# Optimization experiments

Hardware: AMD Instinct MI355X
Metric: run time of the kernel (lower is better)

Reference implementation:

```python
import jax, jax.numpy as jnp
import numpy as np

N_NODES = 10000
N_EDGES = 160000
IN_F = 16
D = 512
N_GRAPHS = 64
N_OUT = 18
BN_EPS = 1e-5


def setup_inputs() -> dict:
    key = jax.random.key(0)
    ks = jax.random.split(key, 16)
    inp = {}
    inp["x"] = jax.random.normal(ks[0], (N_NODES, IN_F), dtype=jnp.float32)
    inp["edge_index"] = jax.random.randint(ks[1], (2, N_EDGES), 0, N_NODES, dtype=jnp.int32)
    inp["batch"] = jnp.sort(jax.random.randint(ks[2], (N_NODES,), 0, N_GRAPHS, dtype=jnp.int32))
    s_in = 1.0 / np.sqrt(IN_F)
    s_d = 1.0 / np.sqrt(D)
    # layer 1 MLP (Linear(IN_F,D) -> ReLU -> Linear(D,D))
    inp["W1a"] = jax.random.uniform(ks[3], (IN_F, D), jnp.float32, -s_in, s_in)
    inp["b1a"] = jnp.zeros((D,), jnp.float32)
    inp["W1b"] = jax.random.uniform(ks[4], (D, D), jnp.float32, -s_d, s_d)
    inp["b1b"] = jnp.zeros((D,), jnp.float32)
    # layers 2-5 stacked MLPs
    inp["Wa"] = jax.random.uniform(ks[5], (4, D, D), jnp.float32, -s_d, s_d)
    inp["ba"] = jnp.zeros((4, D), jnp.float32)
    inp["Wb"] = jax.random.uniform(ks[6], (4, D, D), jnp.float32, -s_d, s_d)
    inp["bb"] = jnp.zeros((4, D), jnp.float32)
    # batchnorm affine params for the 5 BN layers
    inp["bn_gamma"] = jnp.ones((5, D), jnp.float32)
    inp["bn_beta"] = jnp.zeros((5, D), jnp.float32)
    # final fc1 and logits head
    inp["Wfc"] = jax.random.uniform(ks[7], (D, D), jnp.float32, -s_d, s_d)
    inp["bfc"] = jnp.zeros((D,), jnp.float32)
    inp["Wlog"] = 0.01 * jax.random.normal(ks[8], (D, N_OUT), jnp.float32)
    inp["blog"] = jnp.zeros((N_OUT,), jnp.float32)
    return inp


def _gin_agg(x, src, dst):
    # GIN with eps=0: (1+eps)*x + sum_{j in N(i)} x_j  (messages src -> dst)
    msg = x[src]  # [E, D] gather
    agg = jax.ops.segment_sum(msg, dst, num_segments=N_NODES)
    return x + agg


def _mlp(h, Wa, ba, Wb, bb):
    return jax.nn.relu(h @ Wa + ba) @ Wb + bb


def _bn(h, gamma, beta):
    # BatchNorm1d training-mode: batch stats over node dim
    mean = jnp.mean(h, axis=0)
    var = jnp.var(h, axis=0)
    return (h - mean) * (gamma * jax.lax.rsqrt(var + BN_EPS)) + beta


def reference(x, edge_index, batch, W1a, b1a, W1b, b1b, Wa, ba, Wb, bb,
              bn_gamma, bn_beta, Wfc, bfc, Wlog, blog):
    src, dst = edge_index[0], edge_index[1]
    # conv1
    h = jax.nn.relu(_mlp(_gin_agg(x, src, dst), W1a, b1a, W1b, b1b))
    h = _bn(h, bn_gamma[0], bn_beta[0])
    # conv2..conv5
    for i in range(4):
        h = jax.nn.relu(_mlp(_gin_agg(h, src, dst), Wa[i], ba[i], Wb[i], bb[i]))
        h = _bn(h, bn_gamma[i + 1], bn_beta[i + 1])
    # global_mean_pool over graphs
    sums = jax.ops.segment_sum(h, batch, num_segments=N_GRAPHS)
    counts = jax.ops.segment_sum(jnp.ones((N_NODES,), jnp.float32), batch, num_segments=N_GRAPHS)
    pooled = sums / jnp.maximum(counts, 1.0)[:, None]  # [G, D]
    feats = jnp.tanh(pooled @ Wfc + bfc)
    logits = feats @ Wlog + blog  # [G, N_OUT]
    return logits
```

## Files before the change

### kernel.cpp

```cpp
#include <hip/hip_runtime.h>

#define NODES 10000
#define EDGES 160000
#define INF_ 16
#define DD 512
#define GRAPHS 64
#define NOUT 18
#define BN_EPS 1e-5f
#define NBUCK 8

using u16 = unsigned short;
typedef __attribute__((ext_vector_type(8))) _Float16 f16x8;
typedef __attribute__((ext_vector_type(4))) float f32x4;

__device__ __forceinline__ float h2f(u16 u) {
  union { u16 u; _Float16 h; } v; v.u = u; return (float)v.h;
}
__device__ __forceinline__ u16 f2h(float f) {
  union { u16 u; _Float16 h; } v; v.h = (_Float16)f; return v.u;
}
__device__ __forceinline__ void add8(uint4 u, float* a) {
  a[0] += h2f((u16)(u.x & 0xffff)); a[1] += h2f((u16)(u.x >> 16));
  a[2] += h2f((u16)(u.y & 0xffff)); a[3] += h2f((u16)(u.y >> 16));
  a[4] += h2f((u16)(u.z & 0xffff)); a[5] += h2f((u16)(u.z >> 16));
  a[6] += h2f((u16)(u.w & 0xffff)); a[7] += h2f((u16)(u.w >> 16));
}
__device__ __forceinline__ unsigned int pk(float a, float b) {
  return (unsigned int)f2h(a) | ((unsigned int)f2h(b) << 16);
}
__device__ __forceinline__ int lower_bound_dev(const int* __restrict__ batch, int g) {
  int lo = 0, hi = NODES;
  while (lo < hi) { int m = (lo + hi) >> 1; if (batch[m] < g) lo = m + 1; else hi = m; }
  return lo;
}
__device__ __forceinline__ int lds_m(int row, int byte) {
  return (row * 1152 + (byte ^ ((row & 7) << 4))) >> 1;
}

__global__ __launch_bounds__(256) void k_prep(int* __restrict__ cur, float* __restrict__ bg,
                                              const float* __restrict__ W1b, const float* __restrict__ Wa,
                                              const float* __restrict__ Wb, u16* __restrict__ Wf) {
  __shared__ float tile[32][33];
  int b = blockIdx.x;
  int t = threadIdx.x;
  if (b < 288) {
    bg[b * 256 + t] = 0.f;
    return;
  }
  if (b < 328) {
    int i = (b - 288) * 256 + t;
    if (i < NODES) cur[i] = 0;
    return;
  }
  int wb = b - 328;
  int nb = wb & 15, kb = (wb >> 4) & 15, z = wb >> 8;
  const float* src = (z == 0) ? W1b : (z <= 4 ? Wa + (size_t)(z - 1) * DD * DD
                                              : Wb + (size_t)(z - 5) * DD * DD);
  int tx = t & 31, ty = t >> 5;
#pragma unroll
  for (int i = 0; i < 4; ++i)
    tile[ty + 8 * i][tx] = src[(size_t)(kb * 32 + ty + 8 * i) * DD + nb * 32 + tx];
  __syncthreads();
  u16* dst = Wf + (size_t)z * 262144;
#pragma unroll
  for (int p = 0; p < 4; ++p) {
    int i = t + 256 * p;
    int ntl = i >> 9;
    int rem = i & 511;
    int kl = ((rem >> 3) & 3) * 8 + (rem & 7);
    int nl = ntl * 16 + (rem >> 5);
    dst[(size_t)((nb * 2 + ntl) * 16 + kb) * 512 + rem] = f2h(tile[kl][nl]);
  }
}

__global__ void k_count(const int* __restrict__ dst, int* __restrict__ cnt) {
  int e = blockIdx.x * 256 + threadIdx.x;
  if (e < EDGES) atomicAdd(&cnt[dst[e]], 1);
}

__global__ __launch_bounds__(1024) void k_scan(int* __restrict__ cnt, int* __restrict__ rowptr) {
  __shared__ int s[1024];
  int t = threadIdx.x;
  int base = t * 10;
  int c[10]; int sum = 0;
#pragma unroll
  for (int i = 0; i < 10; ++i) {
    int idx = base + i;
    c[i] = (idx < NODES) ? cnt[idx] : 0;
    if (idx < NODES) cnt[idx] = 0;
    sum += c[i];
  }
  s[t] = sum; __syncthreads();
  for (int off = 1; off < 1024; off <<= 1) {
    int v = s[t];
    int a = (t >= off) ? s[t - off] : 0;
    __syncthreads();
    s[t] = v + a;
    __syncthreads();
  }
  int run = (t == 0) ? 0 : s[t - 1];
#pragma unroll
  for (int i = 0; i < 10; ++i) { int idx = base + i; if (idx < NODES) rowptr[idx] = run; run += c[i]; }
  if (t == 1023) rowptr[NODES] = s[1023];
}

__global__ void k_fill(const int* __restrict__ src, const int* __restrict__ dst,
                       const int* __restrict__ rowptr, int* __restrict__ cur, int* __restrict__ col) {
  int e = blockIdx.x * 256 + threadIdx.x;
  if (e < EDGES) {
    int d = dst[e];
    int p = atomicAdd(&cur[d], 1);
    col[rowptr[d] + p] = src[e];
  }
}

__global__ __launch_bounds__(256) void k_l1(const float* __restrict__ x, const int* __restrict__ rowptr,
                                            const int* __restrict__ col, const float* __restrict__ W1a,
                                            const float* __restrict__ b1a, u16* __restrict__ out) {
  __shared__ float sh0[16][17];
  int t = threadIdx.x;
  int nl = t >> 4, ch = t & 15;
  int node = blockIdx.x * 16 + nl;
  float acc = x[node * INF_ + ch];
  int r1 = rowptr[node + 1];
  for (int idx = rowptr[node]; idx < r1; ++idx)
    acc += x[col[idx] * INF_ + ch];
  sh0[nl][ch] = acc;
  __syncthreads();
#pragma unroll
  for (int p = 0; p < 2; ++p) {
    int c = t + 256 * p;
    float wreg[16];
#pragma unroll
    for (int k = 0; k < 16; ++k) wreg[k] = W1a[k * DD + c];
    float bv = b1a[c];
#pragma unroll
    for (int r = 0; r < 16; ++r) {
      float s = bv;
#pragma unroll
      for (int k = 0; k < 16; ++k) s = fmaf(sh0[r][k], wreg[k], s);
      out[(size_t)(blockIdx.x * 16 + r) * DD + c] = f2h(fmaxf(s, 0.f));
    }
  }
}

__global__ __launch_bounds__(256) void k_gath(const u16* __restrict__ Hin, const int* __restrict__ rowptr,
                                              const int* __restrict__ col, const float* __restrict__ statsIn,
                                              const float* __restrict__ gamma, const float* __restrict__ beta,
                                              u16* __restrict__ Tout) {
  __shared__ float ssc[512], ssh[512];
  int t = threadIdx.x;
#pragma unroll
  for (int r = 0; r < 2; ++r) {
    int c = t + r * 256;
    float s = 0.f, qv = 0.f;
#pragma unroll
    for (int b = 0; b < NBUCK; ++b) {
      s += statsIn[b * 1024 + c];
      qv += statsIn[b * 1024 + 512 + c];
    }
    float mean = s * (1.f / NODES);
    float var = qv * (1.f / NODES) - mean * mean;
    float sc = gamma[c] * rsqrtf(var + BN_EPS);
    ssc[c] = sc;
    ssh[c] = beta[c] - mean * sc;
  }
  __syncthreads();

  int lane = t & 63;
  int node = blockIdx.x * 4 + (t >> 6);
  int c8 = lane * 8;
  const u16* hp = Hin + c8;
  float4 scA = *(const float4*)(ssc + c8), scB = *(const float4*)(ssc + c8 + 4);
  float4 shA = *(const float4*)(ssh + c8), shB = *(const float4*)(ssh + c8 + 4);
  float acc[8];
  {
    uint4 sv = *(const uint4*)(hp + (size_t)node * DD);
    acc[0] = h2f((u16)(sv.x & 0xffff)); acc[1] = h2f((u16)(sv.x >> 16));
    acc[2] = h2f((u16)(sv.y & 0xffff)); acc[3] = h2f((u16)(sv.y >> 16));
    acc[4] = h2f((u16)(sv.z & 0xffff)); acc[5] = h2f((u16)(sv.z >> 16));
    acc[6] = h2f((u16)(sv.w & 0xffff)); acc[7] = h2f((u16)(sv.w >> 16));
  }
  int r0 = rowptr[node], r1 = rowptr[node + 1];
  int idx = r0;
  for (; idx + 7 < r1; idx += 8) {
    int j0 = col[idx], j1 = col[idx + 1], j2 = col[idx + 2], j3 = col[idx + 3];
    int j4 = col[idx + 4], j5 = col[idx + 5], j6 = col[idx + 6], j7 = col[idx + 7];
    uint4 a = *(const uint4*)(hp + (size_t)j0 * DD);
    uint4 b = *(const uint4*)(hp + (size_t)j1 * DD);
    uint4 c = *(const uint4*)(hp + (size_t)j2 * DD);
    uint4 d = *(const uint4*)(hp + (size_t)j3 * DD);
    uint4 e = *(const uint4*)(hp + (size_t)j4 * DD);
    uint4 f = *(const uint4*)(hp + (size_t)j5 * DD);
    uint4 g = *(const uint4*)(hp + (size_t)j6 * DD);
    uint4 h = *(const uint4*)(hp + (size_t)j7 * DD);
    add8(a, acc); add8(b, acc); add8(c, acc); add8(d, acc);
    add8(e, acc); add8(f, acc); add8(g, acc); add8(h, acc);
  }
  for (; idx + 3 < r1; idx += 4) {
    int j0 = col[idx], j1 = col[idx + 1], j2 = col[idx + 2], j3 = col[idx + 3];
    uint4 a = *(const uint4*)(hp + (size_t)j0 * DD);
    uint4 b = *(const uint4*)(hp + (size_t)j1 * DD);
    uint4 c = *(const uint4*)(hp + (size_t)j2 * DD);
    uint4 d = *(const uint4*)(hp + (size_t)j3 * DD);
    add8(a, acc); add8(b, acc); add8(c, acc); add8(d, acc);
  }
  for (; idx < r1; ++idx) {
    uint4 a = *(const uint4*)(hp + (size_t)col[idx] * DD);
    add8(a, acc);
  }
  float nn = (float)(r1 - r0 + 1);
  uint4 o;
  o.x = pk(scA.x * acc[0] + nn * shA.x, scA.y * acc[1] + nn * shA.y);
  o.y = pk(scA.z * acc[2] + nn * shA.z, scA.w * acc[3] + nn * shA.w);
  o.z = pk(scB.x * acc[4] + nn * shB.x, scB.y * acc[5] + nn * shB.y);
  o.w = pk(scB.z * acc[6] + nn * shB.z, scB.w * acc[7] + nn * shB.w);
  *(uint4*)(Tout + (size_t)node * DD + c8) = o;
}

__device__ __forceinline__ void gemm_tile(const u16* At, const u16* __restrict__ Wz,
                                          int wave, int q, int r16, f32x4 (&acc)[4][2]) {
  const u16* wp = Wz + (size_t)(wave * 2) * 16 * 512 + (r16 * 4 + q) * 8;
#pragma unroll
  for (int ks = 0; ks < 16; ++ks) {
    f16x8 af[4], bh[2];
#pragma unroll
    for (int mt = 0; mt < 4; ++mt)
      af[mt] = *(const f16x8*)(At + lds_m(mt * 16 + r16, ks * 64 + q * 16));
#pragma unroll
    for (int nt = 0; nt < 2; ++nt)
      bh[nt] = *(const f16x8*)(wp + (size_t)(nt * 16 + ks) * 512);
#pragma unroll
    for (int mt = 0; mt < 4; ++mt)
#pragma unroll
      for (int nt = 0; nt < 2; ++nt)
        acc[mt][nt] = __builtin_amdgcn_mfma_f32_16x16x32_f16(af[mt], bh[nt], acc[mt][nt], 0, 0, 0);
  }
}

template <int TWO>
__global__ __launch_bounds__(1024, 4) void k_mlp(const u16* __restrict__ Ag,
    const u16* __restrict__ WzA, const float* __restrict__ bA,
    const u16* __restrict__ WzB, const float* __restrict__ bB,
    u16* __restrict__ Hout, float* __restrict__ statsB) {
  __shared__ __align__(16) u16 At[64 * 576];
  const int T = threadIdx.x;
  const int M0 = blockIdx.x * 64;
#pragma unroll
  for (int p = 0; p < 4; ++p) {
    int idx = p * 1024 + T;
    int row = idx >> 6, cq = idx & 63;
    uint4 v = make_uint4(0u, 0u, 0u, 0u);
    if (M0 + row < NODES) v = *(const uint4*)(Ag + (size_t)(M0 + row) * DD + cq * 8);
    *(uint4*)(At + lds_m(row, cq * 16)) = v;
  }
  __syncthreads();
  const int lane = T & 63, wave = T >> 6;
  const int q = lane >> 4, r16 = lane & 15;
  const int wn = wave * 32;
  if (TWO) {
    f32x4 acc[4][2] = {};
    gemm_tile(At, WzA, wave, q, r16, acc);
    __syncthreads();
#pragma unroll
    for (int nt = 0; nt < 2; ++nt) {
      int c = wn + nt * 16 + r16;
      float bv = bA[c];
#pragma unroll
      for (int mt = 0; mt < 4; ++mt)
#pragma unroll
        for (int rr = 0; rr < 4; ++rr)
          At[lds_m(mt * 16 + q * 4 + rr, c * 2)] = f2h(fmaxf(acc[mt][nt][rr] + bv, 0.f));
    }
    __syncthreads();
  }
  f32x4 acc[4][2] = {};
  gemm_tile(At, WzB, wave, q, r16, acc);
  float colS[2] = {}, colQ[2] = {};
#pragma unroll
  for (int nt = 0; nt < 2; ++nt) {
    int c = wn + nt * 16 + r16;
    float bv = bB[c];
#pragma unroll
    for (int mt = 0; mt < 4; ++mt) {
#pragma unroll
      for (int rr = 0; rr < 4; ++rr) {
        int row = M0 + mt * 16 + q * 4 + rr;
        if (row < NODES) {
          float v = fmaxf(acc[mt][nt][rr] + bv, 0.f);
          Hout[(size_t)row * DD + c] = f2h(v);
          colS[nt] += v; colQ[nt] += v * v;
        }
      }
    }
  }
#pragma unroll
  for (int nt = 0; nt < 2; ++nt) {
    colS[nt] += __shfl_xor(colS[nt], 16); colS[nt] += __shfl_xor(colS[nt], 32);
    colQ[nt] += __shfl_xor(colQ[nt], 16); colQ[nt] += __shfl_xor(colQ[nt], 32);
  }
  if (q == 0) {
    float* sb = statsB + (size_t)(blockIdx.x & (NBUCK - 1)) * 1024;
#pragma unroll
    for (int nt = 0; nt < 2; ++nt) {
      int c = wn + nt * 16 + r16;
      atomicAdd(&sb[c], colS[nt]);
      atomicAdd(&sb[512 + c], colQ[nt]);
    }
  }
}

__global__ __launch_bounds__(128) void k_pool_part(const u16* __restrict__ h, const int* __restrict__ batch,
                                                   float* __restrict__ gsum) {
  int g = blockIdx.x;
  int s = blockIdx.y;
  int c4 = threadIdx.x * 4;
  int r0 = lower_bound_dev(batch, g);
  int r1 = lower_bound_dev(batch, g + 1);
  int cnt = r1 - r0;
  int len = (cnt + 7) >> 3;
  int rs = r0 + s * len;
  int re = min(rs + len, r1);
  if (rs >= re) return;
  float4 acc = make_float4(0.f, 0.f, 0.f, 0.f);
  for (int r = rs; r < re; ++r) {
    ushort4 v = *(const ushort4*)(h + (size_t)r * DD + c4);
    acc.x += h2f(v.x); acc.y += h2f(v.y); acc.z += h2f(v.z); acc.w += h2f(v.w);
  }
  atomicAdd(&gsum[g * DD + c4 + 0], acc.x);
  atomicAdd(&gsum[g * DD + c4 + 1], acc.y);
  atomicAdd(&gsum[g * DD + c4 + 2], acc.z);
  atomicAdd(&gsum[g * DD + c4 + 3], acc.w);
}

__global__ __launch_bounds__(256) void k_headf(const float* __restrict__ gsum, const int* __restrict__ batch,
                                               const float* __restrict__ stats,
                                               const float* __restrict__ gamma, const float* __restrict__ beta,
                                               const float* __restrict__ Wfc, const float* __restrict__ bfc,
                                               float* __restrict__ feats) {
  __shared__ float pv[512];
  __shared__ float red[4][64];
  int g = blockIdx.x;
  int t = threadIdx.x;
  int r0 = lower_bound_dev(batch, g);
  int r1 = lower_bound_dev(batch, g + 1);
  float inv = 1.f / fmaxf((float)(r1 - r0), 1.f);
#pragma unroll
  for (int r = 0; r < 2; ++r) {
    int c = t + r * 256;
    float s = 0.f, qv = 0.f;
#pragma unroll
    for (int b = 0; b < NBUCK; ++b) {
      s += stats[b * 1024 + c];
      qv += stats[b * 1024 + 512 + c];
    }
    float mean = s * (1.f / NODES);
    float var = qv * (1.f / NODES) - mean * mean;
    float sc = gamma[c] * rsqrtf(var + BN_EPS);
    float sh = beta[c] - mean * sc;
    pv[c] = gsum[g * DD + c] * inv * sc + sh;
  }
  __syncthreads();
  int colc = blockIdx.y * 64 + (t & 63);
  int kc = t >> 6;
  float p = 0.f;
  int k0 = kc * 128;
  for (int k = k0; k < k0 + 128; ++k)
    p = fmaf(pv[k], Wfc[k * DD + colc], p);
  red[kc][t & 63] = p;
  __syncthreads();
  if (t < 64) {
    int c = blockIdx.y * 64 + t;
    float v = red[0][t] + red[1][t] + red[2][t] + red[3][t] + bfc[c];
    feats[g * DD + c] = tanhf(v);
  }
}

__global__ __launch_bounds__(64) void k_logits2(const float* __restrict__ feats, const float* __restrict__ Wlog,
                                                const float* __restrict__ blog, float* __restrict__ out) {
  int g = blockIdx.x, o = blockIdx.y;
  int lane = threadIdx.x;
  float p = 0.f;
  for (int k = lane; k < DD; k += 64)
    p = fmaf(feats[g * DD + k], Wlog[k * NOUT + o], p);
#pragma unroll
  for (int off = 32; off > 0; off >>= 1)
    p += __shfl_down(p, off);
  if (lane == 0) out[g * NOUT + o] = p + blog[o];
}

extern "C" void kernel_launch(void* const* d_in, const int* in_sizes, int n_in,
                              void* d_out, int out_size, void* d_ws, size_t ws_size,
                              hipStream_t stream) {
  const float* x = (const float*)d_in[0];
  const int* ei = (const int*)d_in[1];
  const int* batch = (const int*)d_in[2];
  const float* W1a = (const float*)d_in[3];
  const float* b1a = (const float*)d_in[4];
  const float* W1b = (const float*)d_in[5];
  const float* b1b = (const float*)d_in[6];
  const float* Wa = (const float*)d_in[7];
  const float* ba = (const float*)d_in[8];
  const float* Wb = (const float*)d_in[9];
  const float* bb = (const float*)d_in[10];
  const float* bng = (const float*)d_in[11];
  const float* bnb = (const float*)d_in[12];
  const float* Wfc = (const float*)d_in[13];
  const float* bfc = (const float*)d_in[14];
  const float* Wlog = (const float*)d_in[15];
  const float* blog = (const float*)d_in[16];
  float* out = (float*)d_out;

  const int* src = ei;
  const int* dstp = ei + EDGES;

  char* w = (char*)d_ws;
  int* rowptr  = (int*)(w);
  int* cur     = (int*)(w + 40192);
  int* col     = (int*)(w + 80384);
  float* bns   = (float*)(w + 720384);
  float* gsum  = (float*)(w + 884224);
  float* feats = (float*)(w + 1015296);
  u16* Wf      = (u16*)(w + 1146368);
  u16* H0      = (u16*)(w + 5864960);
  u16* H1      = (u16*)(w + 16104960);

  k_prep<<<2632, 256, 0, stream>>>(cur, bns, W1b, Wa, Wb, Wf);
  k_count<<<625, 256, 0, stream>>>(dstp, cur);
  k_scan<<<1, 1024, 0, stream>>>(cur, rowptr);
  k_fill<<<625, 256, 0, stream>>>(src, dstp, rowptr, cur, col);

  k_l1<<<625, 256, 0, stream>>>(x, rowptr, col, W1a, b1a, H1);
  k_mlp<0><<<157, 1024, 0, stream>>>(H1, nullptr, nullptr, Wf, b1b, H0, bns);

  for (int i = 0; i < 4; ++i) {
    k_gath<<<2500, 256, 0, stream>>>(H0, rowptr, col, bns + (size_t)i * 8192,
                                     bng + i * DD, bnb + i * DD, H1);
    k_mlp<1><<<157, 1024, 0, stream>>>(H1,
        Wf + (size_t)(1 + i) * 262144, ba + i * DD,
        Wf + (size_t)(5 + i) * 262144, bb + i * DD,
        H0, bns + (size_t)(i + 1) * 8192);
  }

  k_pool_part<<<dim3(GRAPHS, 8), 128, 0, stream>>>(H0, batch, gsum);
  k_headf<<<dim3(GRAPHS, 8), 256, 0, stream>>>(gsum, batch, bns + (size_t)4 * 8192,
                                               bng + 4 * DD, bnb + 4 * DD, Wfc, bfc, feats);
  k_logits2<<<dim3(GRAPHS, NOUT), 64, 0, stream>>>(feats, Wlog, blog, out);
}
```

Baseline: 395.8 us.

## Split gather across column blocks and hoist BN scale/shift into separate kernel

The neighbor-gather kernel now uses a 2D grid in which each block handles one 128-column slice, and each lane loads 2 halves (4 bytes) per neighbor instead of 16 bytes. The per-block BatchNorm statistic reduction moves into a tiny single-block kernel that writes scale/shift arrays, so each gather block no longer recomputes them. This gives more blocks and less per-thread work and redundancy, at the cost of narrower 4-byte loads, index and rowptr reads repeated four times, and an extra launch per layer.

After: 414.6 us. 1.05x slower.

```diff
diff --git a/kernel.cpp b/kernel.cpp
--- a/kernel.cpp
+++ b/kernel.cpp
@@ -10,6 +10,7 @@
 #define NBUCK 8
 
 using u16 = unsigned short;
+using u32 = unsigned int;
 typedef __attribute__((ext_vector_type(8))) _Float16 f16x8;
 typedef __attribute__((ext_vector_type(4))) float f32x4;
 
@@ -18,12 +19,6 @@
 }
 __device__ __forceinline__ u16 f2h(float f) {
   union { u16 u; _Float16 h; } v; v.h = (_Float16)f; return v.u;
-}
-__device__ __forceinline__ void add8(uint4 u, float* a) {
-  a[0] += h2f((u16)(u.x & 0xffff)); a[1] += h2f((u16)(u.x >> 16));
-  a[2] += h2f((u16)(u.y & 0xffff)); a[3] += h2f((u16)(u.y >> 16));
-  a[4] += h2f((u16)(u.z & 0xffff)); a[5] += h2f((u16)(u.z >> 16));
-  a[6] += h2f((u16)(u.w & 0xffff)); a[7] += h2f((u16)(u.w >> 16));
 }
 __device__ __forceinline__ unsigned int pk(float a, float b) {
   return (unsigned int)f2h(a) | ((unsigned int)f2h(b) << 16);
@@ -144,78 +139,58 @@
   }
 }
 
+__global__ __launch_bounds__(512) void k_bnf(const float* __restrict__ statsIn,
+                                             const float* __restrict__ gamma, const float* __restrict__ beta,
+                                             float* __restrict__ scf, float* __restrict__ shf) {
+  int c = threadIdx.x;
+  float s = 0.f, qv = 0.f;
+#pragma unroll
+  for (int b = 0; b < NBUCK; ++b) {
+    s += statsIn[b * 1024 + c];
+    qv += statsIn[b * 1024 + 512 + c];
+  }
+  float mean = s * (1.f / NODES);
+  float var = qv * (1.f / NODES) - mean * mean;
+  float sc = gamma[c] * rsqrtf(var + BN_EPS);
+  scf[c] = sc;
+  shf[c] = beta[c] - mean * sc;
+}
+
 __global__ __launch_bounds__(256) void k_gath(const u16* __restrict__ Hin, const int* __restrict__ rowptr,
-                                              const int* __restrict__ col, const float* __restrict__ statsIn,
-                                              const float* __restrict__ gamma, const float* __restrict__ beta,
-                                              u16* __restrict__ Tout) {
-  __shared__ float ssc[512], ssh[512];
+                                              const int* __restrict__ col, const float* __restrict__ scf,
+                                              const float* __restrict__ shf, u16* __restrict__ Tout) {
   int t = threadIdx.x;
-#pragma unroll
-  for (int r = 0; r < 2; ++r) {
-    int c = t + r * 256;
-    float s = 0.f, qv = 0.f;
-#pragma unroll
-    for (int b = 0; b < NBUCK; ++b) {
-      s += statsIn[b * 1024 + c];
-      qv += statsIn[b * 1024 + 512 + c];
-    }
-    float mean = s * (1.f / NODES);
-    float var = qv * (1.f / NODES) - mean * mean;
-    float sc = gamma[c] * rsqrtf(var + BN_EPS);
-    ssc[c] = sc;
-    ssh[c] = beta[c] - mean * sc;
-  }
-  __syncthreads();
-
-  int lane = t & 63;
-  int node = blockIdx.x * 4 + (t >> 6);
-  int c8 = lane * 8;
-  const u16* hp = Hin + c8;
-  float4 scA = *(const float4*)(ssc + c8), scB = *(const float4*)(ssc + c8 + 4);
-  float4 shA = *(const float4*)(ssh + c8), shB = *(const float4*)(ssh + c8 + 4);
-  float acc[8];
+  int lane = t & 63, wave = t >> 6;
+  int node = blockIdx.x * 4 + wave;
+  int c = blockIdx.y * 128 + lane * 2;
+  float2 scv = *(const float2*)(scf + c);
+  float2 shv = *(const float2*)(shf + c);
+  const u16* hp = Hin + c;
+  float a0, a1;
   {
-    uint4 sv = *(const uint4*)(hp + (size_t)node * DD);
-    acc[0] = h2f((u16)(sv.x & 0xffff)); acc[1] = h2f((u16)(sv.x >> 16));
-    acc[2] = h2f((u16)(sv.y & 0xffff)); acc[3] = h2f((u16)(sv.y >> 16));
-    acc[4] = h2f((u16)(sv.z & 0xffff)); acc[5] = h2f((u16)(sv.z >> 16));
-    acc[6] = h2f((u16)(sv.w & 0xffff)); acc[7] = h2f((u16)(sv.w >> 16));
+    u32 sv = *(const u32*)(hp + (size_t)node * DD);
+    a0 = h2f((u16)(sv & 0xffff)); a1 = h2f((u16)(sv >> 16));
   }
   int r0 = rowptr[node], r1 = rowptr[node + 1];
   int idx = r0;
-  for (; idx + 7 < r1; idx += 8) {
-    int j0 = col[idx], j1 = col[idx + 1], j2 = col[idx + 2], j3 = col[idx + 3];
-    int j4 = col[idx + 4], j5 = col[idx + 5], j6 = col[idx + 6], j7 = col[idx + 7];
-    uint4 a = *(const uint4*)(hp + (size_t)j0 * DD);
-    uint4 b = *(const uint4*)(hp + (size_t)j1 * DD);
-    uint4 c = *(const uint4*)(hp + (size_t)j2 * DD);
-    uint4 d = *(const uint4*)(hp + (size_t)j3 * DD);
-    uint4 e = *(const uint4*)(hp + (size_t)j4 * DD);
-    uint4 f = *(const uint4*)(hp + (size_t)j5 * DD);
-    uint4 g = *(const uint4*)(hp + (size_t)j6 * DD);
-    uint4 h = *(const uint4*)(hp + (size_t)j7 * DD);
-    add8(a, acc); add8(b, acc); add8(c, acc); add8(d, acc);
-    add8(e, acc); add8(f, acc); add8(g, acc); add8(h, acc);
-  }
   for (; idx + 3 < r1; idx += 4) {
     int j0 = col[idx], j1 = col[idx + 1], j2 = col[idx + 2], j3 = col[idx + 3];
-    uint4 a = *(const uint4*)(hp + (size_t)j0 * DD);
-    uint4 b = *(const uint4*)(hp + (size_t)j1 * DD);
-    uint4 c = *(const uint4*)(hp + (size_t)j2 * DD);
-    uint4 d = *(const uint4*)(hp + (size_t)j3 * DD);
-    add8(a, acc); add8(b, acc); add8(c, acc); add8(d, acc);
+    u32 v0 = *(const u32*)(hp + (size_t)j0 * DD);
+    u32 v1 = *(const u32*)(hp + (size_t)j1 * DD);
+    u32 v2 = *(const u32*)(hp + (size_t)j2 * DD);
+    u32 v3 = *(const u32*)(hp + (size_t)j3 * DD);
+    a0 += h2f((u16)(v0 & 0xffff)); a1 += h2f((u16)(v0 >> 16));
+    a0 += h2f((u16)(v1 & 0xffff)); a1 += h2f((u16)(v1 >> 16));
+    a0 += h2f((u16)(v2 & 0xffff)); a1 += h2f((u16)(v2 >> 16));
+    a0 += h2f((u16)(v3 & 0xffff)); a1 += h2f((u16)(v3 >> 16));
   }
   for (; idx < r1; ++idx) {
-    uint4 a = *(const uint4*)(hp + (size_t)col[idx] * DD);
-    add8(a, acc);
+    u32 v = *(const u32*)(hp + (size_t)col[idx] * DD);
+    a0 += h2f((u16)(v & 0xffff)); a1 += h2f((u16)(v >> 16));
   }
   float nn = (float)(r1 - r0 + 1);
-  uint4 o;
-  o.x = pk(scA.x * acc[0] + nn * shA.x, scA.y * acc[1] + nn * shA.y);
-  o.y = pk(scA.z * acc[2] + nn * shA.z, scA.w * acc[3] + nn * shA.w);
-  o.z = pk(scB.x * acc[4] + nn * shB.x, scB.y * acc[5] + nn * shB.y);
-  o.w = pk(scB.z * acc[6] + nn * shB.z, scB.w * acc[7] + nn * shB.w);
-  *(uint4*)(Tout + (size_t)node * DD + c8) = o;
+  u32 o = pk(scv.x * a0 + nn * shv.x, scv.y * a1 + nn * shv.y);
+  *(u32*)(Tout + (size_t)node * DD + c) = o;
 }
 
 __device__ __forceinline__ void gemm_tile(const u16* At, const u16* __restrict__ Wz,
@@ -421,9 +396,11 @@
   float* bns   = (float*)(w + 720384);
   float* gsum  = (float*)(w + 884224);
   float* feats = (float*)(w + 1015296);
-  u16* Wf      = (u16*)(w + 1146368);
-  u16* H0      = (u16*)(w + 5864960);
-  u16* H1      = (u16*)(w + 16104960);
+  float* scf   = (float*)(w + 1146368);
+  float* shf   = (float*)(w + 1148416);
+  u16* Wf      = (u16*)(w + 1150464);
+  u16* H0      = (u16*)(w + 5869056);
+  u16* H1      = (u16*)(w + 16109056);
 
   k_prep<<<2632, 256, 0, stream>>>(cur, bns, W1b, Wa, Wb, Wf);
   k_count<<<625, 256, 0, stream>>>(dstp, cur);
@@ -434,8 +411,8 @@
   k_mlp<0><<<157, 1024, 0, stream>>>(H1, nullptr, nullptr, Wf, b1b, H0, bns);
 
   for (int i = 0; i < 4; ++i) {
-    k_gath<<<2500, 256, 0, stream>>>(H0, rowptr, col, bns + (size_t)i * 8192,
-                                     bng + i * DD, bnb + i * DD, H1);
+    k_bnf<<<1, 512, 0, stream>>>(bns + (size_t)i * 8192, bng + i * DD, bnb + i * DD, scf, shf);
+    k_gath<<<dim3(2500, 4), 256, 0, stream>>>(H0, rowptr, col, scf, shf, H1);
     k_mlp<1><<<157, 1024, 0, stream>>>(H1,
         Wf + (size_t)(1 + i) * 262144, ba + i * DD,
         Wf + (size_t)(5 + i) * 262144, bb + i * DD,
```

## Fuse neighbor gather and BN-apply into the MLP GEMM kernel

Applied to the files above, without the earlier changes.

Merges the layer-1 aggregation and first linear into the second-GEMM kernel, and fuses each layer's gather+BN-apply into its two-GEMM MLP kernel, writing aggregated rows straight into LDS. This removes the intermediate H1 round trip through global memory and cuts the launch count, with output buffers now ping-ponged. The catch is that the gather phase now runs on only 157 blocks of 1024 threads, each wave handling 4 nodes serially, so latency hiding for the random gathers is much lower than with the 2500-block standalone kernel.

Result: faster. 370.1 us (-6.5%).

```diff
diff --git a/kernel.cpp b/kernel.cpp
--- a/kernel.cpp
+++ b/kernel.cpp
@@ -10,6 +10,7 @@
 #define NBUCK 8
 
 using u16 = unsigned short;
+using u32 = unsigned int;
 typedef __attribute__((ext_vector_type(8))) _Float16 f16x8;
 typedef __attribute__((ext_vector_type(4))) float f32x4;
 
@@ -114,110 +115,6 @@
   }
 }
 
-__global__ __launch_bounds__(256) void k_l1(const float* __restrict__ x, const int* __restrict__ rowptr,
-                                            const int* __restrict__ col, const float* __restrict__ W1a,
-                                            const float* __restrict__ b1a, u16* __restrict__ out) {
-  __shared__ float sh0[16][17];
-  int t = threadIdx.x;
-  int nl = t >> 4, ch = t & 15;
-  int node = blockIdx.x * 16 + nl;
-  float acc = x[node * INF_ + ch];
-  int r1 = rowptr[node + 1];
-  for (int idx = rowptr[node]; idx < r1; ++idx)
-    acc += x[col[idx] * INF_ + ch];
-  sh0[nl][ch] = acc;
-  __syncthreads();
-#pragma unroll
-  for (int p = 0; p < 2; ++p) {
-    int c = t + 256 * p;
-    float wreg[16];
-#pragma unroll
-    for (int k = 0; k < 16; ++k) wreg[k] = W1a[k * DD + c];
-    float bv = b1a[c];
-#pragma unroll
-    for (int r = 0; r < 16; ++r) {
-      float s = bv;
-#pragma unroll
-      for (int k = 0; k < 16; ++k) s = fmaf(sh0[r][k], wreg[k], s);
-      out[(size_t)(blockIdx.x * 16 + r) * DD + c] = f2h(fmaxf(s, 0.f));
-    }
-  }
-}
-
-__global__ __launch_bounds__(256) void k_gath(const u16* __restrict__ Hin, const int* __restrict__ rowptr,
-                                              const int* __restrict__ col, const float* __restrict__ statsIn,
-                                              const float* __restrict__ gamma, const float* __restrict__ beta,
-                                              u16* __restrict__ Tout) {
-  __shared__ float ssc[512], ssh[512];
-  int t = threadIdx.x;
-#pragma unroll
-  for (int r = 0; r < 2; ++r) {
-    int c = t + r * 256;
-    float s = 0.f, qv = 0.f;
-#pragma unroll
-    for (int b = 0; b < NBUCK; ++b) {
-      s += statsIn[b * 1024 + c];
-      qv += statsIn[b * 1024 + 512 + c];
-    }
-    float mean = s * (1.f / NODES);
-    float var = qv * (1.f / NODES) - mean * mean;
-    float sc = gamma[c] * rsqrtf(var + BN_EPS);
-    ssc[c] = sc;
-    ssh[c] = beta[c] - mean * sc;
-  }
-  __syncthreads();
-
-  int lane = t & 63;
-  int node = blockIdx.x * 4 + (t >> 6);
-  int c8 = lane * 8;
-  const u16* hp = Hin + c8;
-  float4 scA = *(const float4*)(ssc + c8), scB = *(const float4*)(ssc + c8 + 4);
-  float4 shA = *(const float4*)(ssh + c8), shB = *(const float4*)(ssh + c8 + 4);
-  float acc[8];
-  {
-    uint4 sv = *(const uint4*)(hp + (size_t)node * DD);
-    acc[0] = h2f((u16)(sv.x & 0xffff)); acc[1] = h2f((u16)(sv.x >> 16));
-    acc[2] = h2f((u16)(sv.y & 0xffff)); acc[3] = h2f((u16)(sv.y >> 16));
-    acc[4] = h2f((u16)(sv.z & 0xffff)); acc[5] = h2f((u16)(sv.z >> 16));
-    acc[6] = h2f((u16)(sv.w & 0xffff)); acc[7] = h2f((u16)(sv.w >> 16));
-  }
-  int r0 = rowptr[node], r1 = rowptr[node + 1];
-  int idx = r0;
-  for (; idx + 7 < r1; idx += 8) {
-    int j0 = col[idx], j1 = col[idx + 1], j2 = col[idx + 2], j3 = col[idx + 3];
-    int j4 = col[idx + 4], j5 = col[idx + 5], j6 = col[idx + 6], j7 = col[idx + 7];
-    uint4 a = *(const uint4*)(hp + (size_t)j0 * DD);
-    uint4 b = *(const uint4*)(hp + (size_t)j1 * DD);
-    uint4 c = *(const uint4*)(hp + (size_t)j2 * DD);
-    uint4 d = *(const uint4*)(hp + (size_t)j3 * DD);
-    uint4 e = *(const uint4*)(hp + (size_t)j4 * DD);
-    uint4 f = *(const uint4*)(hp + (size_t)j5 * DD);
-    uint4 g = *(const uint4*)(hp + (size_t)j6 * DD);
-    uint4 h = *(const uint4*)(hp + (size_t)j7 * DD);
-    add8(a, acc); add8(b, acc); add8(c, acc); add8(d, acc);
-    add8(e, acc); add8(f, acc); add8(g, acc); add8(h, acc);
-  }
-  for (; idx + 3 < r1; idx += 4) {
-    int j0 = col[idx], j1 = col[idx + 1], j2 = col[idx + 2], j3 = col[idx + 3];
-    uint4 a = *(const uint4*)(hp + (size_t)j0 * DD);
-    uint4 b = *(const uint4*)(hp + (size_t)j1 * DD);
-    uint4 c = *(const uint4*)(hp + (size_t)j2 * DD);
-    uint4 d = *(const uint4*)(hp + (size_t)j3 * DD);
-    add8(a, acc); add8(b, acc); add8(c, acc); add8(d, acc);
-  }
-  for (; idx < r1; ++idx) {
-    uint4 a = *(const uint4*)(hp + (size_t)col[idx] * DD);
-    add8(a, acc);
-  }
-  float nn = (float)(r1 - r0 + 1);
-  uint4 o;
-  o.x = pk(scA.x * acc[0] + nn * shA.x, scA.y * acc[1] + nn * shA.y);
-  o.y = pk(scA.z * acc[2] + nn * shA.z, scA.w * acc[3] + nn * shA.w);
-  o.z = pk(scB.x * acc[4] + nn * shB.x, scB.y * acc[5] + nn * shB.y);
-  o.w = pk(scB.z * acc[6] + nn * shB.z, scB.w * acc[7] + nn * shB.w);
-  *(uint4*)(Tout + (size_t)node * DD + c8) = o;
-}
-
 __device__ __forceinline__ void gemm_tile(const u16* At, const u16* __restrict__ Wz,
                                           int wave, int q, int r16, f32x4 (&acc)[4][2]) {
   const u16* wp = Wz + (size_t)(wave * 2) * 16 * 512 + (r16 * 4 + q) * 8;
@@ -238,44 +135,10 @@
   }
 }
 
-template <int TWO>
-__global__ __launch_bounds__(1024, 4) void k_mlp(const u16* __restrict__ Ag,
-    const u16* __restrict__ WzA, const float* __restrict__ bA,
-    const u16* __restrict__ WzB, const float* __restrict__ bB,
-    u16* __restrict__ Hout, float* __restrict__ statsB) {
-  __shared__ __align__(16) u16 At[64 * 576];
-  const int T = threadIdx.x;
-  const int M0 = blockIdx.x * 64;
-#pragma unroll
-  for (int p = 0; p < 4; ++p) {
-    int idx = p * 1024 + T;
-    int row = idx >> 6, cq = idx & 63;
-    uint4 v = make_uint4(0u, 0u, 0u, 0u);
-    if (M0 + row < NODES) v = *(const uint4*)(Ag + (size_t)(M0 + row) * DD + cq * 8);
-    *(uint4*)(At + lds_m(row, cq * 16)) = v;
-  }
-  __syncthreads();
-  const int lane = T & 63, wave = T >> 6;
-  const int q = lane >> 4, r16 = lane & 15;
+__device__ __forceinline__ void gemm_out(f32x4 (&acc)[4][2], const float* __restrict__ bB,
+                                         u16* __restrict__ Hout, float* __restrict__ sb,
+                                         int M0, int wave, int q, int r16) {
   const int wn = wave * 32;
-  if (TWO) {
-    f32x4 acc[4][2] = {};
-    gemm_tile(At, WzA, wave, q, r16, acc);
-    __syncthreads();
-#pragma unroll
-    for (int nt = 0; nt < 2; ++nt) {
-      int c = wn + nt * 16 + r16;
-      float bv = bA[c];
-#pragma unroll
-      for (int mt = 0; mt < 4; ++mt)
-#pragma unroll
-        for (int rr = 0; rr < 4; ++rr)
-          At[lds_m(mt * 16 + q * 4 + rr, c * 2)] = f2h(fmaxf(acc[mt][nt][rr] + bv, 0.f));
-    }
-    __syncthreads();
-  }
-  f32x4 acc[4][2] = {};
-  gemm_tile(At, WzB, wave, q, r16, acc);
   float colS[2] = {}, colQ[2] = {};
 #pragma unroll
   for (int nt = 0; nt < 2; ++nt) {
@@ -300,7 +163,6 @@
     colQ[nt] += __shfl_xor(colQ[nt], 16); colQ[nt] += __shfl_xor(colQ[nt], 32);
   }
   if (q == 0) {
-    float* sb = statsB + (size_t)(blockIdx.x & (NBUCK - 1)) * 1024;
 #pragma unroll
     for (int nt = 0; nt < 2; ++nt) {
       int c = wn + nt * 16 + r16;
@@ -308,6 +170,157 @@
       atomicAdd(&sb[512 + c], colQ[nt]);
     }
   }
+}
+
+__global__ __launch_bounds__(1024, 4) void k_l1m(const float* __restrict__ x,
+    const int* __restrict__ rowptr, const int* __restrict__ col,
+    const float* __restrict__ W1a, const float* __restrict__ b1a,
+    const u16* __restrict__ WzB, const float* __restrict__ bB,
+    u16* __restrict__ Hout, float* __restrict__ statsOut) {
+  __shared__ float T0[64][17];
+  __shared__ __align__(16) u16 At[64 * 576];
+  const int T = threadIdx.x;
+  const int M0 = blockIdx.x * 64;
+  {
+    int nl = T >> 4, ch = T & 15;
+    int node = M0 + nl;
+    float acc = 0.f;
+    if (node < NODES) {
+      acc = x[(size_t)node * INF_ + ch];
+      int r1 = rowptr[node + 1];
+      for (int idx = rowptr[node]; idx < r1; ++idx)
+        acc += x[(size_t)col[idx] * INF_ + ch];
+    }
+    T0[nl][ch] = acc;
+  }
+  __syncthreads();
+  {
+    int c = T & 511;
+    int h = T >> 9;
+    float wreg[16];
+#pragma unroll
+    for (int k = 0; k < 16; ++k) wreg[k] = W1a[k * DD + c];
+    float bv = b1a[c];
+    for (int r = h * 32; r < h * 32 + 32; ++r) {
+      float s = bv;
+#pragma unroll
+      for (int k = 0; k < 16; ++k) s = fmaf(T0[r][k], wreg[k], s);
+      At[lds_m(r, c * 2)] = f2h(fmaxf(s, 0.f));
+    }
+  }
+  __syncthreads();
+  const int lane = T & 63, wave = T >> 6;
+  const int q = lane >> 4, r16 = lane & 15;
+  f32x4 acc[4][2] = {};
+  gemm_tile(At, WzB, wave, q, r16, acc);
+  gemm_out(acc, bB, Hout, statsOut + (size_t)(blockIdx.x & (NBUCK - 1)) * 1024,
+           M0, wave, q, r16);
+}
+
+__global__ __launch_bounds__(1024, 4) void k_fused(
+    const u16* __restrict__ Hin, const int* __restrict__ rowptr, const int* __restrict__ col,
+    const float* __restrict__ statsIn, const float* __restrict__ gamma, const float* __restrict__ beta,
+    const u16* __restrict__ WzA, const float* __restrict__ bA,
+    const u16* __restrict__ WzB, const float* __restrict__ bB,
+    u16* __restrict__ Hout, float* __restrict__ statsOut) {
+  __shared__ float ssc[512], ssh[512];
+  __shared__ __align__(16) u16 At[64 * 576];
+  const int T = threadIdx.x;
+  const int M0 = blockIdx.x * 64;
+  if (T < 512) {
+    int c = T;
+    float s = 0.f, qv = 0.f;
+#pragma unroll
+    for (int b = 0; b < NBUCK; ++b) {
+      s += statsIn[b * 1024 + c];
+      qv += statsIn[b * 1024 + 512 + c];
+    }
+    float mean = s * (1.f / NODES);
+    float var = qv * (1.f / NODES) - mean * mean;
+    float sc = gamma[c] * rsqrtf(var + BN_EPS);
+    ssc[c] = sc;
+    ssh[c] = beta[c] - mean * sc;
+  }
+  __syncthreads();
+  const int lane = T & 63, wave = T >> 6;
+  const int c8 = lane * 8;
+  const u16* hp = Hin + c8;
+  float4 scA = *(const float4*)(ssc + c8), scB = *(const float4*)(ssc + c8 + 4);
+  float4 shA = *(const float4*)(ssh + c8), shB = *(const float4*)(ssh + c8 + 4);
+  for (int ps = 0; ps < 4; ++ps) {
+    int nl = wave * 4 + ps;
+    int node = M0 + nl;
+    if (node < NODES) {
+      float acc[8];
+      {
+        uint4 sv = *(const uint4*)(hp + (size_t)node * DD);
+        acc[0] = h2f((u16)(sv.x & 0xffff)); acc[1] = h2f((u16)(sv.x >> 16));
+        acc[2] = h2f((u16)(sv.y & 0xffff)); acc[3] = h2f((u16)(sv.y >> 16));
+        acc[4] = h2f((u16)(sv.z & 0xffff)); acc[5] = h2f((u16)(sv.z >> 16));
+        acc[6] = h2f((u16)(sv.w & 0xffff)); acc[7] = h2f((u16)(sv.w >> 16));
+      }
+      int r0 = rowptr[node], r1 = rowptr[node + 1];
+      int idx = r0;
+      for (; idx + 7 < r1; idx += 8) {
+        int j0 = col[idx], j1 = col[idx + 1], j2 = col[idx + 2], j3 = col[idx + 3];
+        int j4 = col[idx + 4], j5 = col[idx + 5], j6 = col[idx + 6], j7 = col[idx + 7];
+        uint4 a = *(const uint4*)(hp + (size_t)j0 * DD);
+        uint4 b = *(const uint4*)(hp + (size_t)j1 * DD);
+        uint4 c = *(const uint4*)(hp + (size_t)j2 * DD);
+        uint4 d = *(const uint4*)(hp + (size_t)j3 * DD);
+        uint4 e = *(const uint4*)(hp + (size_t)j4 * DD);
+        uint4 f = *(const uint4*)(hp + (size_t)j5 * DD);
+        uint4 g = *(const uint4*)(hp + (size_t)j6 * DD);
+        uint4 h = *(const uint4*)(hp + (size_t)j7 * DD);
+        add8(a, acc); add8(b, acc); add8(c, acc); add8(d, acc);
+        add8(e, acc); add8(f, acc); add8(g, acc); add8(h, acc);
+      }
+      for (; idx + 3 < r1; idx += 4) {
+        int j0 = col[idx], j1 = col[idx + 1], j2 = col[idx + 2], j3 = col[idx + 3];
+        uint4 a = *(const uint4*)(hp + (size_t)j0 * DD);
+        uint4 b = *(const uint4*)(hp + (size_t)j1 * DD);
+        uint4 c = *(const uint4*)(hp + (size_t)j2 * DD);
+        uint4 d = *(const uint4*)(hp + (size_t)j3 * DD);
+        add8(a, acc); add8(b, acc); add8(c, acc); add8(d, acc);
+      }
+      for (; idx < r1; ++idx) {
+        uint4 a = *(const uint4*)(hp + (size_t)col[idx] * DD);
+        add8(a, acc);
+      }
+      float nn = (float)(r1 - r0 + 1);
+      uint4 o;
+      o.x = pk(scA.x * acc[0] + nn * shA.x, scA.y * acc[1] + nn * shA.y);
+      o.y = pk(scA.z * acc[2] + nn * shA.z, scA.w * acc[3] + nn * shA.w);
+      o.z = pk(scB.x * acc[4] + nn * shB.x, scB.y * acc[5] + nn * shB.y);
+      o.w = pk(scB.z * acc[6] + nn * shB.z, scB.w * acc[7] + nn * shB.w);
+      *(uint4*)(At + lds_m(nl, lane * 16)) = o;
+    } else {
+      *(uint4*)(At + lds_m(nl, lane * 16)) = make_uint4(0u, 0u, 0u, 0u);
+    }
+  }
+  __syncthreads();
+  const int q = lane >> 4, r16 = lane & 15;
+  const int wn = wave * 32;
+  {
+    f32x4 acc[4][2] = {};
+    gemm_tile(At, WzA, wave, q, r16, acc);
+    __syncthreads();
+#pragma unroll
+    for (int nt = 0; nt < 2; ++nt) {
+      int c = wn + nt * 16 + r16;
+      float bv = bA[c];
+#pragma unroll
+      for (int mt = 0; mt < 4; ++mt)
+#pragma unroll
+        for (int rr = 0; rr < 4; ++rr)
+          At[lds_m(mt * 16 + q * 4 + rr, c * 2)] = f2h(fmaxf(acc[mt][nt][rr] + bv, 0.f));
+    }
+    __syncthreads();
+  }
+  f32x4 acc[4][2] = {};
+  gemm_tile(At, WzB, wave, q, r16, acc);
+  gemm_out(acc, bB, Hout, statsOut + (size_t)(blockIdx.x & (NBUCK - 1)) * 1024,
+           M0, wave, q, r16);
 }
 
 __global__ __launch_bounds__(128) void k_pool_part(const u16* __restrict__ h, const int* __restrict__ batch,
@@ -430,19 +443,20 @@
   k_scan<<<1, 1024, 0, stream>>>(cur, rowptr);
   k_fill<<<625, 256, 0, stream>>>(src, dstp, rowptr, cur, col);
 
-  k_l1<<<625, 256, 0, stream>>>(x, rowptr, col, W1a, b1a, H1);
-  k_mlp<0><<<157, 1024, 0, stream>>>(H1, nullptr, nullptr, Wf, b1b, H0, bns);
-
+  k_l1m<<<157, 1024, 0, stream>>>(x, rowptr, col, W1a, b1a, Wf, b1b, H0, bns);
+
+  u16* Hin = H0;
+  u16* Ho = H1;
   for (int i = 0; i < 4; ++i) {
-    k_gath<<<2500, 256, 0, stream>>>(H0, rowptr, col, bns + (size_t)i * 8192,
-                                     bng + i * DD, bnb + i * DD, H1);
-    k_mlp<1><<<157, 1024, 0, stream>>>(H1,
+    k_fused<<<157, 1024, 0, stream>>>(Hin, rowptr, col, bns + (size_t)i * 8192,
+        bng + i * DD, bnb + i * DD,
         Wf + (size_t)(1 + i) * 262144, ba + i * DD,
         Wf + (size_t)(5 + i) * 262144, bb + i * DD,
-        H0, bns + (size_t)(i + 1) * 8192);
-  }
-
-  k_pool_part<<<dim3(GRAPHS, 8), 128, 0, stream>>>(H0, batch, gsum);
+        Ho, bns + (size_t)(i + 1) * 8192);
+    u16* tmp = Hin; Hin = Ho; Ho = tmp;
+  }
+
+  k_pool_part<<<dim3(GRAPHS, 8), 128, 0, stream>>>(Hin, batch, gsum);
   k_headf<<<dim3(GRAPHS, 8), 256, 0, stream>>>(gsum, batch, bns + (size_t)4 * 8192,
                                                bng + 4 * DD, bnb + 4 * DD, Wfc, bfc, feats);
   k_logits2<<<dim3(GRAPHS, NOUT), 64, 0, stream>>>(feats, Wlog, blog, out);
```
